# Optimization experiments

Measured on AMD Instinct MI355X. Metric: run time of the kernel, lower is better.

## Reference

```python
import jax, jax.numpy as jnp
import numpy as np


def _leaky(x):
    return jnp.where(x > 0, x, 0.2 * x)


def _time_warp(x, strength, k_wp, k_sh):
    # Vectorized equivalent of the per-sample python loop in _apply_time_warp.
    B, L, Fd = x.shape
    warp_steps = (L * 0.1 * strength).astype(jnp.int32)
    wp = jax.random.randint(k_wp, (B, 1), warp_steps, L - warp_steps)
    sh = jax.random.randint(k_sh, (B, 1), -warp_steps, warp_steps + 1)
    t = jnp.arange(L)[None, :]
    # shift > 0: warped[t] = x[min(t+shift, L-1)] for t >= warp_point, else x[t]
    pos = jnp.where(t >= wp, jnp.minimum(t + sh, L - 1), t)
    # shift < 0: warped[t] = x[t - shift] for warp_point+shift <= t < L+shift, else x[t]
    neg = jnp.where((t >= wp + sh) & (t < L + sh), t - sh, t)
    idx = jnp.where(sh > 0, pos, jnp.where(sh < 0, neg, t))  # (B, L)
    warped = x[jnp.arange(B)[:, None], idx]  # gather along time -> (B, L, Fd)
    return warped


def _freq_aug(x, strength, k_f):
    fx = jnp.fft.fft(x, axis=1)
    ratio = jnp.minimum(strength * 0.1, 0.5)
    keep = jax.random.uniform(k_f, x.shape) > ratio
    res = jnp.fft.ifft(fx * keep.astype(fx.dtype), axis=1).real.astype(x.dtype)
    return jnp.where(strength < 0.01, x, res)


def _forward(x, batch_size, w1, b1, w2, b2, w3, b3, wm, bm, wn, bn, ws, bs,
             p_mask, p_noise, p_shift, p_scale):
    B, L, Fd = x.shape
    s_mask = jax.nn.sigmoid(p_mask)
    s_noise = jax.nn.sigmoid(p_noise)
    s_shift = jax.nn.sigmoid(p_shift)
    s_scale = jax.nn.sigmoid(p_scale)
    s_mix = 1.0 - s_shift

    key = jax.random.key(42)
    kz, kn, kwp, ksh, kf = jax.random.split(key, 5)

    z = jax.random.normal(kz, (B, w1.shape[0]), x.dtype)
    h = _leaky(z @ w1 + b1)
    h = _leaky(h @ w2 + b2)
    h = _leaky(h @ w3 + b3)  # (B, 2*hidden)

    mask = jax.nn.sigmoid(h @ wm + bm).reshape(B, L, Fd)
    mask = 1.0 - (1.0 - mask) * s_mask * 0.3

    noise_mag = jax.nn.softplus(h @ wn + bn).reshape(B, L, Fd)
    noise = jax.random.normal(kn, x.shape, x.dtype) * noise_mag * s_noise * 0.05

    warped = _time_warp(x, s_shift, kwp, ksh)

    scale = jax.nn.softplus(h @ ws + bs)[:, None, :]  # (B,1,Fd)
    scale = 1.0 + (scale - 0.5) * 0.2 * s_scale

    freq = _freq_aug(x, s_mix, kf)

    wa = jnp.clip(1.0 - s_mix - s_shift, 0.1, 0.8)
    wb = s_mix * 0.5
    wc = s_shift * 0.5
    tot = wa + wb + wc
    wa, wb, wc = wa / tot, wb / tot, wc / tot

    aug = x * mask * scale + noise
    aug = aug * wa + freq * wb + warped * wc
    return aug


def setup_inputs() -> dict:
    key = jax.random.key(0)
    ks = jax.random.split(key, 8)
    B, L, Fd = 256, 512, 64
    H, ND = 128, 64
    x = jax.random.normal(ks[0], (B, L, Fd), jnp.float32)

    def lin(k, i, o):
        return jax.random.normal(k, (i, o), jnp.float32) * 0.02

    inp = {
        "x": x,
        "batch_size": B,
        "w1": lin(ks[1], ND, H), "b1": jnp.zeros((H,), jnp.float32),
        "w2": lin(ks[2], H, 2 * H), "b2": jnp.zeros((2 * H,), jnp.float32),
        "w3": lin(ks[3], 2 * H, 2 * H), "b3": jnp.zeros((2 * H,), jnp.float32),
        "wm": lin(ks[4], 2 * H, L * Fd), "bm": jnp.zeros((L * Fd,), jnp.float32),
        "wn": lin(ks[5], 2 * H, L * Fd), "bn": jnp.zeros((L * Fd,), jnp.float32),
        "ws": lin(ks[6], 2 * H, Fd), "bs": jnp.zeros((Fd,), jnp.float32),
        "p_mask": jnp.float32(0.5), "p_noise": jnp.float32(0.5),
        "p_shift": jnp.float32(0.5), "p_scale": jnp.float32(0.5),
    }
    return inp


def reference(x, batch_size, w1, b1, w2, b2, w3, b3, wm, bm, wn, bn, ws, bs,
              p_mask, p_noise, p_shift, p_scale):
    return _forward(x, batch_size, w1, b1, w2, b2, w3, b3, wm, bm, wn, bn,
                    ws, bs, p_mask, p_noise, p_shift, p_scale)
```

## Files before the change

kernel.cpp:

```cpp
#include <hip/hip_runtime.h>
#include <cstdint>
#include <cstddef>


typedef unsigned int u32;
typedef unsigned short u16;

#define Bd 256
#define Ld 512
#define Fd 64
#define Nd 32768

struct U2 { u32 a, b; };

__device__ __forceinline__ u32 rotl32(u32 x, int r){ return (x << r) | (x >> (32 - r)); }

__device__ __forceinline__ U2 tf2x32(u32 k0, u32 k1, u32 x0, u32 x1){
  u32 ks2 = k0 ^ k1 ^ 0x1BD11BDAu;
  x0 += k0; x1 += k1;
#define TFR4(r0,r1,r2,r3) \
  x0 += x1; x1 = rotl32(x1, r0); x1 ^= x0; \
  x0 += x1; x1 = rotl32(x1, r1); x1 ^= x0; \
  x0 += x1; x1 = rotl32(x1, r2); x1 ^= x0; \
  x0 += x1; x1 = rotl32(x1, r3); x1 ^= x0;
  TFR4(13,15,26,6)  x0 += k1;  x1 += ks2 + 1u;
  TFR4(17,29,16,24) x0 += ks2; x1 += k0 + 2u;
  TFR4(13,15,26,6)  x0 += k0;  x1 += k1 + 3u;
  TFR4(17,29,16,24) x0 += k1;  x1 += ks2 + 4u;
  TFR4(13,15,26,6)  x0 += ks2; x1 += k0 + 5u;
#undef TFR4
  U2 r; r.a = x0; r.b = x1; return r;
}

__device__ __forceinline__ u32 rb32(u32 k0, u32 k1, u32 i){
  U2 r = tf2x32(k0, k1, 0u, i);
  return r.a ^ r.b;
}

__device__ __forceinline__ U2 split_key(u32 k0, u32 k1, u32 j){
  return tf2x32(k0, k1, 0u, j);
}

__device__ __forceinline__ float sigmoidf_(float x){ return 1.0f / (1.0f + expf(-x)); }
__device__ __forceinline__ float softplusf_(float x){ return fmaxf(x, 0.0f) + log1pf(expf(-fabsf(x))); }
__device__ __forceinline__ float leakyf_(float x){ return (x > 0.0f) ? x : 0.2f * x; }

__device__ __forceinline__ float erfinvf_(float x){
  float w = -log1pf(-x * x);
  float p;
  if (w < 5.0f){
    w -= 2.5f;
    p =               2.81022636e-08f;
    p = fmaf(p, w,    3.43273939e-07f);
    p = fmaf(p, w,   -3.5233877e-06f);
    p = fmaf(p, w,   -4.39150654e-06f);
    p = fmaf(p, w,    0.00021858087f);
    p = fmaf(p, w,   -0.00125372503f);
    p = fmaf(p, w,   -0.00417768164f);
    p = fmaf(p, w,    0.246640727f);
    p = fmaf(p, w,    1.50140941f);
  } else {
    w = sqrtf(w) - 3.0f;
    p =              -0.000200214257f;
    p = fmaf(p, w,    0.000100950558f);
    p = fmaf(p, w,    0.00134934322f);
    p = fmaf(p, w,   -0.00367342844f);
    p = fmaf(p, w,    0.00573950773f);
    p = fmaf(p, w,   -0.0076224613f);
    p = fmaf(p, w,    0.00943887047f);
    p = fmaf(p, w,    1.00167406f);
    p = fmaf(p, w,    2.83297682f);
  }
  return p * x;
}

__device__ __forceinline__ float uniform_from_bits(u32 bits){
  return __uint_as_float((bits >> 9) | 0x3f800000u) - 1.0f;
}

__device__ __forceinline__ float normal_from_bits(u32 bits){
  float u01 = uniform_from_bits(bits);
  const float lo = -0.99999994f;
  float v = fmaf(u01, 2.0f, lo);
  v = fmaxf(lo, v);
  return 1.41421356f * erfinvf_(v);
}

__device__ __forceinline__ int warp_idx_(int t, int wp, int sh){
  int tps = t + sh;
  int pos = (t >= wp) ? ((tps < Ld - 1) ? tps : (Ld - 1)) : t;
  int neg = ((t >= wp + sh) && (t < Ld + sh)) ? (t - sh) : t;
  return (sh > 0) ? pos : ((sh < 0) ? neg : t);
}

__device__ __forceinline__ u32 pack_bf16_2(float a, float b){
  u32 ua = __float_as_uint(a), ub = __float_as_uint(b);
  u32 ra = (ua + 0x7FFFu + ((ua >> 16) & 1u)) >> 16;
  u32 rb = (ub + 0x7FFFu + ((ub >> 16) & 1u)) >> 16;
  return (ra & 0xFFFFu) | (rb << 16);
}
__device__ __forceinline__ u16 f2bf(float a){
  u32 ua = __float_as_uint(a);
  return (u16)((ua + 0x7FFFu + ((ua >> 16) & 1u)) >> 16);
}
__device__ __forceinline__ float bf2f(u16 v){
  return __uint_as_float(((u32)v) << 16);
}

__device__ __forceinline__ int swz_(int v){
  return ((v >> 2) & 7) ^ ((v & 3) << 1);
}
__device__ __forceinline__ int rev9_(int k){
  return (int)(__brev((u32)k) >> 23);
}

__global__ __launch_bounds__(256) void k_init(float* __restrict__ z, int* __restrict__ wp,
                                              int* __restrict__ shv, const float* __restrict__ p_shift){
  int gid = blockIdx.x * 256 + threadIdx.x;
  U2 kz = split_key(0u, 42u, 0u);
  z[gid] = normal_from_bits(rb32(kz.a, kz.b, (u32)gid));
  if (blockIdx.x == 0){
    int b = threadIdx.x;
    float s_shift = sigmoidf_(p_shift[0]);
    int wsteps = (int)(51.2f * s_shift);
    U2 kwp = split_key(0u, 42u, 2u);
    U2 ksh = split_key(0u, 42u, 3u);
    {
      U2 k1 = split_key(kwp.a, kwp.b, 0u);
      U2 k2 = split_key(kwp.a, kwp.b, 1u);
      u32 hi = rb32(k1.a, k1.b, (u32)b);
      u32 lo = rb32(k2.a, k2.b, (u32)b);
      u32 span = (u32)(Ld - 2 * wsteps);
      u32 mult = 65536u % span; mult = (mult * mult) % span;
      u32 off = ((hi % span) * mult + (lo % span)) % span;
      wp[b] = wsteps + (int)off;
    }
    {
      U2 k1 = split_key(ksh.a, ksh.b, 0u);
      U2 k2 = split_key(ksh.a, ksh.b, 1u);
      u32 hi = rb32(k1.a, k1.b, (u32)b);
      u32 lo = rb32(k2.a, k2.b, (u32)b);
      u32 span = (u32)(2 * wsteps + 1);
      u32 mult = 65536u % span; mult = (mult * mult) % span;
      u32 off = ((hi % span) * mult + (lo % span)) % span;
      shv[b] = -wsteps + (int)off;
    }
  }
}

__global__ __launch_bounds__(128) void k_mlp1(const float* __restrict__ z, const float* __restrict__ w1,
                                              const float* __restrict__ b1, float* __restrict__ h1){
  int b = blockIdx.x, n = threadIdx.x;
  const float* zr = z + b * 64;
  float acc = b1[n];
  #pragma unroll 8
  for (int k = 0; k < 64; ++k) acc = fmaf(zr[k], w1[k * 128 + n], acc);
  h1[b * 128 + n] = leakyf_(acc);
}

__global__ __launch_bounds__(256) void k_mlp2(const float* __restrict__ h1, const float* __restrict__ w2,
                                              const float* __restrict__ b2, float* __restrict__ h2){
  int b = blockIdx.x, n = threadIdx.x;
  const float* hr = h1 + b * 128;
  float acc = b2[n];
  #pragma unroll 8
  for (int k = 0; k < 128; ++k) acc = fmaf(hr[k], w2[k * 256 + n], acc);
  h2[b * 256 + n] = leakyf_(acc);
}

__global__ __launch_bounds__(256) void k_mlp3(const float* __restrict__ h2, const float* __restrict__ w3,
                                              const float* __restrict__ b3, u16* __restrict__ h3b){
  int b = blockIdx.x, n = threadIdx.x;
  const float* hr = h2 + b * 256;
  float acc = b3[n];
  #pragma unroll 8
  for (int k = 0; k < 256; ++k) acc = fmaf(hr[k], w3[k * 256 + n], acc);
  h3b[b * 256 + n] = f2bf(leakyf_(acc));
}

__global__ __launch_bounds__(256) void k_scale(const u16* __restrict__ h3b, const float* __restrict__ wsc,
                                               const float* __restrict__ bsc, const float* __restrict__ p_scale,
                                               float* __restrict__ scl){
  int tid = threadIdx.x;
  int b = blockIdx.x * 4 + (tid >> 6);
  int f = tid & 63;
  float acc = bsc[f];
  for (int k = 0; k < 256; ++k) acc = fmaf(bf2f(h3b[b * 256 + k]), wsc[k * 64 + f], acc);
  float s_scale = sigmoidf_(p_scale[0]);
  scl[b * 64 + f] = 1.0f + (softplusf_(acc) - 0.5f) * 0.2f * s_scale;
}

typedef short short8 __attribute__((ext_vector_type(8)));
typedef float f32x4 __attribute__((ext_vector_type(4)));
union Frag { uint4 u; short8 s; };

__global__ __launch_bounds__(256, 2) void k_gemm(
    const u16* __restrict__ h3b,
    const float* __restrict__ wm, const float* __restrict__ bm,
    const float* __restrict__ wn, const float* __restrict__ bn,
    u16* __restrict__ logM, u16* __restrict__ logN)
{
  __shared__ __align__(16) u32 As [128 * 32];
  __shared__ __align__(16) u32 Bs0[128 * 32];
  __shared__ __align__(16) u32 Bs1[128 * 32];

  const int tid  = threadIdx.x;
  const int lane = tid & 63;
  const int w    = tid >> 6;
  const int q    = lane >> 4;
  const int lo   = lane & 15;
  const int nt0  = blockIdx.x << 7;
  const int b0   = blockIdx.y << 7;
  const int wr   = (w >> 1) << 6;
  const int wc   = (w & 1) << 6;

  const int p  = lane >> 3;
  const int c8 = lane & 7;
  const int nb = (w << 5) + (p << 2);

  f32x4 accm[4][4], accn[4][4];
  #pragma unroll
  for (int i = 0; i < 4; ++i)
    #pragma unroll
    for (int j = 0; j < 4; ++j){ accm[i][j] = (f32x4)0.0f; accn[i][j] = (f32x4)0.0f; }

  for (int kc = 0; kc < 256; kc += 64){
    if (kc) __syncthreads();
    #pragma unroll
    for (int j = 0; j < 4; ++j){
      int idx  = j * 256 + tid;
      int row  = idx >> 3;
      int slot = idx & 7;
      int g    = slot ^ swz_(row);
      uint4 v  = *(const uint4*)(h3b + (size_t)(b0 + row) * 256 + kc + g * 8);
      *(uint4*)&As[row * 32 + slot * 4] = v;
    }
    #pragma unroll
    for (int cp = 0; cp < 4; ++cp){
      int c = cp * 8 + c8;
      size_t gb = (size_t)(kc + 2 * c) * Nd + nt0 + nb;
      float4 m0 = *(const float4*)(wm + gb);
      float4 m1 = *(const float4*)(wm + gb + Nd);
      float4 v0 = *(const float4*)(wn + gb);
      float4 v1 = *(const float4*)(wn + gb + Nd);
      int g = c >> 2, cl = c & 3;
      #pragma unroll
      for (int s = 0; s < 4; ++s){
        int n = nb + s;
        int addr = n * 32 + (g ^ swz_(n)) * 4 + cl;
        float a0 = (s == 0) ? m0.x : (s == 1) ? m0.y : (s == 2) ? m0.z : m0.w;
        float a1 = (s == 0) ? m1.x : (s == 1) ? m1.y : (s == 2) ? m1.z : m1.w;
        float b0f = (s == 0) ? v0.x : (s == 1) ? v0.y : (s == 2) ? v0.z : v0.w;
        float b1f = (s == 0) ? v1.x : (s == 1) ? v1.y : (s == 2) ? v1.z : v1.w;
        Bs0[addr] = pack_bf16_2(a0, a1);
        Bs1[addr] = pack_bf16_2(b0f, b1f);
      }
    }
    __syncthreads();

    #pragma unroll
    for (int u = 0; u < 2; ++u){
      int G = u * 4 + q;
      Frag af[4], bfm[4], bfn[4];
      #pragma unroll
      for (int mt = 0; mt < 4; ++mt){
        int row = wr + mt * 16 + lo;
        af[mt].u = *(const uint4*)&As[row * 32 + (G ^ swz_(row)) * 4];
      }
      #pragma unroll
      for (int nt = 0; nt < 4; ++nt){
        int n = wc + nt * 16 + lo;
        int ad = n * 32 + (G ^ swz_(n)) * 4;
        bfm[nt].u = *(const uint4*)&Bs0[ad];
        bfn[nt].u = *(const uint4*)&Bs1[ad];
      }
      #pragma unroll
      for (int mt = 0; mt < 4; ++mt){
        #pragma unroll
        for (int nt = 0; nt < 4; ++nt){
          accm[mt][nt] = __builtin_amdgcn_mfma_f32_16x16x32_bf16(af[mt].s, bfm[nt].s, accm[mt][nt], 0, 0, 0);
          accn[mt][nt] = __builtin_amdgcn_mfma_f32_16x16x32_bf16(af[mt].s, bfn[nt].s, accn[mt][nt], 0, 0, 0);
        }
      }
    }
  }

  #pragma unroll
  for (int nt = 0; nt < 4; ++nt){
    int n = nt0 + wc + nt * 16 + lo;
    float bmv = bm[n];
    float bnv = bn[n];
    #pragma unroll
    for (int mt = 0; mt < 4; ++mt){
      #pragma unroll
      for (int r = 0; r < 4; ++r){
        int b = b0 + wr + mt * 16 + q * 4 + r;
        size_t o = (size_t)b * Nd + n;
        logM[o] = f2bf(accm[mt][nt][r] + bmv);
        logN[o] = f2bf(accn[mt][nt][r] + bnv);
      }
    }
  }
}

#define PITCH 529

__device__ __forceinline__ int lphys(int t){ return t + (t >> 5); }

__global__ __launch_bounds__(256, 4) void k_faug(
    const float* __restrict__ x,
    const u16* __restrict__ logM, const u16* __restrict__ logN,
    const float* __restrict__ scl,
    const int* __restrict__ wp, const int* __restrict__ shv,
    const float* __restrict__ p_mask, const float* __restrict__ p_noise,
    const float* __restrict__ p_shift,
    float* __restrict__ out)
{
  __shared__ float SR[8 * PITCH];
  __shared__ float SI[8 * PITCH];
  __shared__ float2 tw[256];

  const int tid = threadIdx.x;
  const int b   = blockIdx.x >> 2;
  const int f0  = (blockIdx.x & 3) << 4;

  float s_mask  = sigmoidf_(p_mask[0]);
  float s_noise = sigmoidf_(p_noise[0]);
  float s_shift = sigmoidf_(p_shift[0]);
  float s_mix   = 1.0f - s_shift;
  float ratio   = fminf(s_mix * 0.1f, 0.5f);
  float wa = 1.0f - s_mix - s_shift;
  wa = fminf(fmaxf(wa, 0.1f), 0.8f);
  float wb = s_mix * 0.5f;
  float wc = s_shift * 0.5f;
  float tot = wa + wb + wc;
  wa /= tot; wb /= tot; wc /= tot;
  bool pass = (s_mix < 0.01f);

  U2 kf  = split_key(0u, 42u, 4u);
  U2 knk = split_key(0u, 42u, 1u);
  const int wpb = wp[b];
  const int shb = shv[b];

  {
    float ang = -6.283185307179586f * ((float)tid / 512.0f);
    tw[tid] = make_float2(cosf(ang), sinf(ang));
  }

  const float* xb = x + (size_t)b * Nd;
  #pragma unroll
  for (int s = 0; s < 8; ++s){
    int qq = (s << 8) + tid;
    int t  = qq >> 2;
    int f4 = qq & 3;
    float4 v = *(const float4*)(xb + t * 64 + f0 + (f4 << 2));
    int j = f4 << 1;
    int pt = lphys(t);
    SR[j * PITCH + pt]       = v.x;  SI[j * PITCH + pt]       = v.y;
    SR[(j + 1) * PITCH + pt] = v.z;  SI[(j + 1) * PITCH + pt] = v.w;
  }
  __syncthreads();

  for (int s = 9; s >= 1; --s){
    int half = 1 << (s - 1);
    #pragma unroll
    for (int it = 0; it < 8; ++it){
      int j  = it;
      int bi = tid;
      int pos = bi & (half - 1);
      int g = bi >> (s - 1);
      int i1 = (g << s) + pos;
      int i2 = i1 + half;
      int a1 = j * PITCH + lphys(i1);
      int a2 = j * PITCH + lphys(i2);
      float ur = SR[a1], ui = SI[a1];
      float vr = SR[a2], vi = SI[a2];
      SR[a1] = ur + vr; SI[a1] = ui + vi;
      float dr = ur - vr, di = ui - vi;
      float2 w = tw[pos << (9 - s)];
      SR[a2] = dr * w.x - di * w.y;
      SI[a2] = dr * w.y + di * w.x;
    }
    __syncthreads();
  }

  #pragma unroll
  for (int it = 0; it < 8; ++it){
    int j = it;
    int k = tid;
    int nItr = (k == 0) ? 2 : 1;
    for (int e = 0; e < nItr; ++e){
      int kk = (e == 0) ? k : 256;
      int nk = (512 - kk) & 511;
      int pk = rev9_(kk), pn = rev9_(nk);
      int ak = j * PITCH + lphys(pk);
      int an = j * PITCH + lphys(pn);
      float zkr = SR[ak], zki = SI[ak];
      float znr = SR[an], zni = SI[an];
      float X0r = 0.5f * (zkr + znr), X0i = 0.5f * (zki - zni);
      float X1r = 0.5f * (zki + zni), X1i = 0.5f * (znr - zkr);
      int fA = f0 + (j << 1);
      u32 ck = (u32)((b * Ld + kk) * Fd + fA);
      u32 cn = (u32)((b * Ld + nk) * Fd + fA);
      float k0a = (uniform_from_bits(rb32(kf.a, kf.b, ck))      > ratio) ? 1.0f : 0.0f;
      float k0b = (uniform_from_bits(rb32(kf.a, kf.b, cn))      > ratio) ? 1.0f : 0.0f;
      float k1a = (uniform_from_bits(rb32(kf.a, kf.b, ck + 1u)) > ratio) ? 1.0f : 0.0f;
      float k1b = (uniform_from_bits(rb32(kf.a, kf.b, cn + 1u)) > ratio) ? 1.0f : 0.0f;
      float m0 = 0.5f * (k0a + k0b);
      float m1 = 0.5f * (k1a + k1b);
      SR[ak] = m0 * X0r - m1 * X1i;
      SI[ak] = m0 * X0i + m1 * X1r;
      SR[an] = m0 * X0r + m1 * X1i;
      SI[an] = m1 * X1r - m0 * X0i;
    }
  }
  __syncthreads();

  for (int s = 1; s <= 9; ++s){
    int half = 1 << (s - 1);
    #pragma unroll
    for (int it = 0; it < 8; ++it){
      int j  = it;
      int bi = tid;
      int pos = bi & (half - 1);
      int g = bi >> (s - 1);
      int i1 = (g << s) + pos;
      int i2 = i1 + half;
      int a1 = j * PITCH + lphys(i1);
      int a2 = j * PITCH + lphys(i2);
      float2 w = tw[pos << (9 - s)];
      float vr = SR[a2], vi = SI[a2];
      float tx_ = vr * w.x + vi * w.y;
      float ty_ = vi * w.x - vr * w.y;
      float ur = SR[a1], ui = SI[a1];
      SR[a1] = ur + tx_; SI[a1] = ui + ty_;
      SR[a2] = ur - tx_; SI[a2] = ui - ty_;
    }
    __syncthreads();
  }

  const float inv512 = 1.0f / 512.0f;
  const u16* lMb = logM + (size_t)b * Nd;
  const u16* lNb = logN + (size_t)b * Nd;
  float* ob = out + (size_t)b * Nd;
  #pragma unroll
  for (int s = 0; s < 8; ++s){
    int qq = (s << 8) + tid;
    int t  = qq >> 2;
    int f4 = qq & 3;
    int f  = f0 + (f4 << 2);
    int j  = f4 << 1;
    int pt = lphys(t);
    int nidx = t * 64 + f;
    float4 xv = *(const float4*)(xb + nidx);
    int wi = warp_idx_(t, wpb, shb);
    float4 wv = *(const float4*)(xb + wi * 64 + f);
    float4 sc = *(const float4*)(scl + b * 64 + f);
    ushort4 mr = *(const ushort4*)(lMb + nidx);
    ushort4 nr4 = *(const ushort4*)(lNb + nidx);
    float fr[4];
    fr[0] = SR[j * PITCH + pt] * inv512;
    fr[1] = SI[j * PITCH + pt] * inv512;
    fr[2] = SR[(j + 1) * PITCH + pt] * inv512;
    fr[3] = SI[(j + 1) * PITCH + pt] * inv512;
    const float xvv[4] = {xv.x, xv.y, xv.z, xv.w};
    const float wvv[4] = {wv.x, wv.y, wv.z, wv.w};
    const float scv[4] = {sc.x, sc.y, sc.z, sc.w};
    const u16 mrv[4] = {mr.x, mr.y, mr.z, mr.w};
    const u16 nrv[4] = {nr4.x, nr4.y, nr4.z, nr4.w};
    float o[4];
    #pragma unroll
    for (int c = 0; c < 4; ++c){
      float maskv = sigmoidf_(bf2f(mrv[c]));
      maskv = 1.0f - (1.0f - maskv) * s_mask * 0.3f;
      float nmag = softplusf_(bf2f(nrv[c]));
      float nz = normal_from_bits(rb32(knk.a, knk.b, (u32)(b * Nd + nidx + c)));
      float noise = nz * nmag * s_noise * 0.05f;
      float fq = pass ? xvv[c] : fr[c];
      float aug = fmaf(xvv[c] * maskv, scv[c], noise);
      o[c] = aug * wa + fq * wb + wvv[c] * wc;
    }
    *(float4*)(ob + nidx) = make_float4(o[0], o[1], o[2], o[3]);
  }
}

extern "C" void kernel_launch(void* const* d_in, const int* in_sizes, int n_in,
                              void* d_out, int out_size, void* d_ws, size_t ws_size,
                              hipStream_t stream)
{
  (void)in_sizes; (void)n_in; (void)out_size; (void)ws_size;
  const float* x   = (const float*)d_in[0];
  const float* w1  = (const float*)d_in[2];
  const float* b1  = (const float*)d_in[3];
  const float* w2  = (const float*)d_in[4];
  const float* b2  = (const float*)d_in[5];
  const float* w3  = (const float*)d_in[6];
  const float* b3  = (const float*)d_in[7];
  const float* wm  = (const float*)d_in[8];
  const float* bm  = (const float*)d_in[9];
  const float* wn  = (const float*)d_in[10];
  const float* bn  = (const float*)d_in[11];
  const float* wsc = (const float*)d_in[12];
  const float* bsc = (const float*)d_in[13];
  const float* pm  = (const float*)d_in[14];
  const float* pn  = (const float*)d_in[15];
  const float* psh = (const float*)d_in[16];
  const float* psc = (const float*)d_in[17];
  float* out = (float*)d_out;
  char* ws = (char*)d_ws;

  int*   wp   = (int*)(ws + 0);
  int*   shv  = (int*)(ws + 1024);
  float* z    = (float*)(ws + 2048);
  float* h1   = (float*)(ws + 67584);
  float* h2   = (float*)(ws + 198656);
  u16*   h3b  = (u16*)  (ws + 460800);
  float* scl  = (float*)(ws + 591872);
  u16*   logM = (u16*)  (ws + 1048576);
  u16*   logN = (u16*)  (ws + 1048576 + 16777216);

  k_init <<<dim3(64),      dim3(256), 0, stream>>>(z, wp, shv, psh);
  k_mlp1 <<<dim3(256),     dim3(128), 0, stream>>>(z, w1, b1, h1);
  k_mlp2 <<<dim3(256),     dim3(256), 0, stream>>>(h1, w2, b2, h2);
  k_mlp3 <<<dim3(256),     dim3(256), 0, stream>>>(h2, w3, b3, h3b);
  k_scale<<<dim3(64),      dim3(256), 0, stream>>>(h3b, wsc, bsc, psc, scl);
  k_gemm <<<dim3(256, 2),  dim3(256), 0, stream>>>(h3b, wm, bm, wn, bn, logM, logN);
  k_faug <<<dim3(1024),    dim3(256), 0, stream>>>(x, logM, logN, scl, wp, shv,
                                                   pm, pn, psh, out);
}
```

Baseline: 327.3 us.

## Fuse MLP chain, pre-pack weights to bf16, move mask/noise epilogue into GEMM

```diff
diff --git a/kernel.cpp b/kernel.cpp
--- a/kernel.cpp
+++ b/kernel.cpp
@@ -99,195 +99,205 @@
   u32 rb = (ub + 0x7FFFu + ((ub >> 16) & 1u)) >> 16;
   return (ra & 0xFFFFu) | (rb << 16);
 }
-__device__ __forceinline__ u16 f2bf(float a){
-  u32 ua = __float_as_uint(a);
-  return (u16)((ua + 0x7FFFu + ((ua >> 16) & 1u)) >> 16);
-}
 __device__ __forceinline__ float bf2f(u16 v){
   return __uint_as_float(((u32)v) << 16);
 }
-
-__device__ __forceinline__ int swz_(int v){
-  return ((v >> 2) & 7) ^ ((v & 3) << 1);
-}
 __device__ __forceinline__ int rev9_(int k){
   return (int)(__brev((u32)k) >> 23);
 }
 
-__global__ __launch_bounds__(256) void k_init(float* __restrict__ z, int* __restrict__ wp,
-                                              int* __restrict__ shv, const float* __restrict__ p_shift){
-  int gid = blockIdx.x * 256 + threadIdx.x;
-  U2 kz = split_key(0u, 42u, 0u);
-  z[gid] = normal_from_bits(rb32(kz.a, kz.b, (u32)gid));
-  if (blockIdx.x == 0){
-    int b = threadIdx.x;
+__global__ __launch_bounds__(256) void k_wprep(const float* __restrict__ wm,
+                                               const float* __restrict__ wn,
+                                               u16* __restrict__ wpk){
+  __shared__ float tile[64 * 260];
+  const int mat = blockIdx.x >> 9;
+  const int s   = blockIdx.x & 511;
+  const int t   = threadIdx.x;
+  const float* src = mat ? wn : wm;
+  const size_t matoff = (size_t)mat * 8388608;
+
+  #pragma unroll
+  for (int r = 0; r < 16; ++r){
+    int k  = r * 16 + (t >> 4);
+    int n4 = (t & 15) << 2;
+    float4 v = *(const float4*)(src + (size_t)k * Nd + s * 64 + n4);
+    tile[(n4 + 0) * 260 + k] = v.x;
+    tile[(n4 + 1) * 260 + k] = v.y;
+    tile[(n4 + 2) * 260 + k] = v.z;
+    tile[(n4 + 3) * 260 + k] = v.w;
+  }
+  __syncthreads();
+
+  const int n = t >> 2, part = t & 3;
+  uint4* dst = (uint4*)(wpk + matoff + (size_t)s * 16384 + n * 256 + part * 64);
+  #pragma unroll
+  for (int u = 0; u < 8; ++u){
+    const float* p = &tile[n * 260 + part * 64 + u * 8];
+    uint4 q;
+    q.x = pack_bf16_2(p[0], p[1]); q.y = pack_bf16_2(p[2], p[3]);
+    q.z = pack_bf16_2(p[4], p[5]); q.w = pack_bf16_2(p[6], p[7]);
+    dst[u] = q;
+  }
+}
+
+__global__ __launch_bounds__(256) void k_pre(
+    const float* __restrict__ w1, const float* __restrict__ b1,
+    const float* __restrict__ w2, const float* __restrict__ b2,
+    const float* __restrict__ w3, const float* __restrict__ b3,
+    const float* __restrict__ wsc, const float* __restrict__ bsc,
+    const float* __restrict__ p_shift, const float* __restrict__ p_scale,
+    uint4* __restrict__ h3p, float* __restrict__ scl,
+    int* __restrict__ wp, int* __restrict__ shv)
+{
+  __shared__ float zs[64], h1s[128], h2s[256], h3s[256];
+  const int b = blockIdx.x;
+  const int t = threadIdx.x;
+
+  if (t < 64){
+    U2 kz = split_key(0u, 42u, 0u);
+    zs[t] = normal_from_bits(rb32(kz.a, kz.b, (u32)(b * 64 + t)));
+  }
+  if (t == 64){
     float s_shift = sigmoidf_(p_shift[0]);
     int wsteps = (int)(51.2f * s_shift);
     U2 kwp = split_key(0u, 42u, 2u);
+    U2 k1 = split_key(kwp.a, kwp.b, 0u);
+    U2 k2 = split_key(kwp.a, kwp.b, 1u);
+    u32 hi = rb32(k1.a, k1.b, (u32)b);
+    u32 lo = rb32(k2.a, k2.b, (u32)b);
+    u32 span = (u32)(Ld - 2 * wsteps);
+    u32 mult = 65536u % span; mult = (mult * mult) % span;
+    u32 off = ((hi % span) * mult + (lo % span)) % span;
+    wp[b] = wsteps + (int)off;
+  }
+  if (t == 65){
+    float s_shift = sigmoidf_(p_shift[0]);
+    int wsteps = (int)(51.2f * s_shift);
     U2 ksh = split_key(0u, 42u, 3u);
-    {
-      U2 k1 = split_key(kwp.a, kwp.b, 0u);
-      U2 k2 = split_key(kwp.a, kwp.b, 1u);
-      u32 hi = rb32(k1.a, k1.b, (u32)b);
-      u32 lo = rb32(k2.a, k2.b, (u32)b);
-      u32 span = (u32)(Ld - 2 * wsteps);
-      u32 mult = 65536u % span; mult = (mult * mult) % span;
-      u32 off = ((hi % span) * mult + (lo % span)) % span;
-      wp[b] = wsteps + (int)off;
-    }
-    {
-      U2 k1 = split_key(ksh.a, ksh.b, 0u);
-      U2 k2 = split_key(ksh.a, ksh.b, 1u);
-      u32 hi = rb32(k1.a, k1.b, (u32)b);
-      u32 lo = rb32(k2.a, k2.b, (u32)b);
-      u32 span = (u32)(2 * wsteps + 1);
-      u32 mult = 65536u % span; mult = (mult * mult) % span;
-      u32 off = ((hi % span) * mult + (lo % span)) % span;
-      shv[b] = -wsteps + (int)off;
-    }
-  }
-}
-
-__global__ __launch_bounds__(128) void k_mlp1(const float* __restrict__ z, const float* __restrict__ w1,
-                                              const float* __restrict__ b1, float* __restrict__ h1){
-  int b = blockIdx.x, n = threadIdx.x;
-  const float* zr = z + b * 64;
-  float acc = b1[n];
-  #pragma unroll 8
-  for (int k = 0; k < 64; ++k) acc = fmaf(zr[k], w1[k * 128 + n], acc);
-  h1[b * 128 + n] = leakyf_(acc);
-}
-
-__global__ __launch_bounds__(256) void k_mlp2(const float* __restrict__ h1, const float* __restrict__ w2,
-                                              const float* __restrict__ b2, float* __restrict__ h2){
-  int b = blockIdx.x, n = threadIdx.x;
-  const float* hr = h1 + b * 128;
-  float acc = b2[n];
-  #pragma unroll 8
-  for (int k = 0; k < 128; ++k) acc = fmaf(hr[k], w2[k * 256 + n], acc);
-  h2[b * 256 + n] = leakyf_(acc);
-}
-
-__global__ __launch_bounds__(256) void k_mlp3(const float* __restrict__ h2, const float* __restrict__ w3,
-                                              const float* __restrict__ b3, u16* __restrict__ h3b){
-  int b = blockIdx.x, n = threadIdx.x;
-  const float* hr = h2 + b * 256;
-  float acc = b3[n];
-  #pragma unroll 8
-  for (int k = 0; k < 256; ++k) acc = fmaf(hr[k], w3[k * 256 + n], acc);
-  h3b[b * 256 + n] = f2bf(leakyf_(acc));
-}
-
-__global__ __launch_bounds__(256) void k_scale(const u16* __restrict__ h3b, const float* __restrict__ wsc,
-                                               const float* __restrict__ bsc, const float* __restrict__ p_scale,
-                                               float* __restrict__ scl){
-  int tid = threadIdx.x;
-  int b = blockIdx.x * 4 + (tid >> 6);
-  int f = tid & 63;
-  float acc = bsc[f];
-  for (int k = 0; k < 256; ++k) acc = fmaf(bf2f(h3b[b * 256 + k]), wsc[k * 64 + f], acc);
-  float s_scale = sigmoidf_(p_scale[0]);
-  scl[b * 64 + f] = 1.0f + (softplusf_(acc) - 0.5f) * 0.2f * s_scale;
+    U2 k1 = split_key(ksh.a, ksh.b, 0u);
+    U2 k2 = split_key(ksh.a, ksh.b, 1u);
+    u32 hi = rb32(k1.a, k1.b, (u32)b);
+    u32 lo = rb32(k2.a, k2.b, (u32)b);
+    u32 span = (u32)(2 * wsteps + 1);
+    u32 mult = 65536u % span; mult = (mult * mult) % span;
+    u32 off = ((hi % span) * mult + (lo % span)) % span;
+    shv[b] = -wsteps + (int)off;
+  }
+  __syncthreads();
+
+  if (t < 128){
+    float acc = b1[t];
+    #pragma unroll 8
+    for (int k = 0; k < 64; ++k) acc = fmaf(zs[k], w1[k * 128 + t], acc);
+    h1s[t] = leakyf_(acc);
+  }
+  __syncthreads();
+  {
+    float acc = b2[t];
+    #pragma unroll 8
+    for (int k = 0; k < 128; ++k) acc = fmaf(h1s[k], w2[k * 256 + t], acc);
+    h2s[t] = leakyf_(acc);
+  }
+  __syncthreads();
+  {
+    float acc = b3[t];
+    #pragma unroll 8
+    for (int k = 0; k < 256; ++k) acc = fmaf(h2s[k], w3[k * 256 + t], acc);
+    h3s[t] = leakyf_(acc);
+  }
+  __syncthreads();
+  if (t < 64){
+    float acc = bsc[t];
+    #pragma unroll 8
+    for (int k = 0; k < 256; ++k) acc = fmaf(h3s[k], wsc[k * 64 + t], acc);
+    float s_scale = sigmoidf_(p_scale[0]);
+    scl[b * 64 + t] = 1.0f + (softplusf_(acc) - 0.5f) * 0.2f * s_scale;
+  }
+  if (t < 32){
+    int c = t;
+    int k0 = (c >> 2) * 32 + (c & 3) * 8;
+    uint4 q;
+    q.x = pack_bf16_2(h3s[k0 + 0], h3s[k0 + 1]);
+    q.y = pack_bf16_2(h3s[k0 + 2], h3s[k0 + 3]);
+    q.z = pack_bf16_2(h3s[k0 + 4], h3s[k0 + 5]);
+    q.w = pack_bf16_2(h3s[k0 + 6], h3s[k0 + 7]);
+    h3p[(b >> 4) * 512 + c * 16 + (b & 15)] = q;
+  }
 }
 
 typedef short short8 __attribute__((ext_vector_type(8)));
 typedef float f32x4 __attribute__((ext_vector_type(4)));
 union Frag { uint4 u; short8 s; };
 
-__global__ __launch_bounds__(256, 2) void k_gemm(
-    const u16* __restrict__ h3b,
-    const float* __restrict__ wm, const float* __restrict__ bm,
-    const float* __restrict__ wn, const float* __restrict__ bn,
-    u16* __restrict__ logM, u16* __restrict__ logN)
+__global__ __launch_bounds__(256) void k_gemm2(
+    const uint4* __restrict__ h3p, const u16* __restrict__ wpk,
+    const float* __restrict__ bm, const float* __restrict__ bn,
+    const float* __restrict__ scl,
+    const float* __restrict__ p_mask, const float* __restrict__ p_noise,
+    u32* __restrict__ mno)
 {
-  __shared__ __align__(16) u32 As [128 * 32];
-  __shared__ __align__(16) u32 Bs0[128 * 32];
-  __shared__ __align__(16) u32 Bs1[128 * 32];
+  __shared__ __align__(16) uint4 Bs[4096];
 
   const int tid  = threadIdx.x;
   const int lane = tid & 63;
   const int w    = tid >> 6;
   const int q    = lane >> 4;
   const int lo   = lane & 15;
-  const int nt0  = blockIdx.x << 7;
+  const int bx   = blockIdx.x;
   const int b0   = blockIdx.y << 7;
-  const int wr   = (w >> 1) << 6;
-  const int wc   = (w & 1) << 6;
-
-  const int p  = lane >> 3;
-  const int c8 = lane & 7;
-  const int nb = (w << 5) + (p << 2);
-
-  f32x4 accm[4][4], accn[4][4];
+  const int wr   = (w & 1) << 6;
+  const int wc   = (w >> 1) << 5;
+
+  #pragma unroll
+  for (int i = 0; i < 16; ++i){
+    int slot = i * 256 + tid;
+    int mat  = slot >> 11;
+    int np   = (slot >> 5) & 63;
+    int gp   = slot & 31;
+    int gi   = gp ^ (np & 7);
+    Bs[slot] = *(const uint4*)(wpk + (size_t)mat * 8388608 +
+                               (size_t)bx * 16384 + np * 256 + gi * 8);
+  }
+  __syncthreads();
+
+  f32x4 accm[4][2], accn[4][2];
   #pragma unroll
   for (int i = 0; i < 4; ++i)
     #pragma unroll
-    for (int j = 0; j < 4; ++j){ accm[i][j] = (f32x4)0.0f; accn[i][j] = (f32x4)0.0f; }
-
-  for (int kc = 0; kc < 256; kc += 64){
-    if (kc) __syncthreads();
-    #pragma unroll
-    for (int j = 0; j < 4; ++j){
-      int idx  = j * 256 + tid;
-      int row  = idx >> 3;
-      int slot = idx & 7;
-      int g    = slot ^ swz_(row);
-      uint4 v  = *(const uint4*)(h3b + (size_t)(b0 + row) * 256 + kc + g * 8);
-      *(uint4*)&As[row * 32 + slot * 4] = v;
-    }
-    #pragma unroll
-    for (int cp = 0; cp < 4; ++cp){
-      int c = cp * 8 + c8;
-      size_t gb = (size_t)(kc + 2 * c) * Nd + nt0 + nb;
-      float4 m0 = *(const float4*)(wm + gb);
-      float4 m1 = *(const float4*)(wm + gb + Nd);
-      float4 v0 = *(const float4*)(wn + gb);
-      float4 v1 = *(const float4*)(wn + gb + Nd);
-      int g = c >> 2, cl = c & 3;
+    for (int j = 0; j < 2; ++j){ accm[i][j] = (f32x4)0.0f; accn[i][j] = (f32x4)0.0f; }
+
+  const int tbase = (blockIdx.y << 3) + ((w & 1) << 2);
+
+  for (int G = 0; G < 8; ++G){
+    Frag af[4], bfm[2], bfn[2];
+    #pragma unroll
+    for (int mt = 0; mt < 4; ++mt)
+      af[mt].u = h3p[(tbase + mt) * 512 + (G * 4 + q) * 16 + lo];
+    #pragma unroll
+    for (int nt = 0; nt < 2; ++nt){
+      int np = wc + nt * 16 + lo;
+      int gp = (G * 4 + q) ^ (np & 7);
+      bfm[nt].u = Bs[np * 32 + gp];
+      bfn[nt].u = Bs[2048 + np * 32 + gp];
+    }
+    #pragma unroll
+    for (int mt = 0; mt < 4; ++mt){
       #pragma unroll
-      for (int s = 0; s < 4; ++s){
-        int n = nb + s;
-        int addr = n * 32 + (g ^ swz_(n)) * 4 + cl;
-        float a0 = (s == 0) ? m0.x : (s == 1) ? m0.y : (s == 2) ? m0.z : m0.w;
-        float a1 = (s == 0) ? m1.x : (s == 1) ? m1.y : (s == 2) ? m1.z : m1.w;
-        float b0f = (s == 0) ? v0.x : (s == 1) ? v0.y : (s == 2) ? v0.z : v0.w;
-        float b1f = (s == 0) ? v1.x : (s == 1) ? v1.y : (s == 2) ? v1.z : v1.w;
-        Bs0[addr] = pack_bf16_2(a0, a1);
-        Bs1[addr] = pack_bf16_2(b0f, b1f);
+      for (int nt = 0; nt < 2; ++nt){
+        accm[mt][nt] = __builtin_amdgcn_mfma_f32_16x16x32_bf16(af[mt].s, bfm[nt].s, accm[mt][nt], 0, 0, 0);
+        accn[mt][nt] = __builtin_amdgcn_mfma_f32_16x16x32_bf16(af[mt].s, bfn[nt].s, accn[mt][nt], 0, 0, 0);
       }
     }
-    __syncthreads();
-
-    #pragma unroll
-    for (int u = 0; u < 2; ++u){
-      int G = u * 4 + q;
-      Frag af[4], bfm[4], bfn[4];
-      #pragma unroll
-      for (int mt = 0; mt < 4; ++mt){
-        int row = wr + mt * 16 + lo;
-        af[mt].u = *(const uint4*)&As[row * 32 + (G ^ swz_(row)) * 4];
-      }
-      #pragma unroll
-      for (int nt = 0; nt < 4; ++nt){
-        int n = wc + nt * 16 + lo;
-        int ad = n * 32 + (G ^ swz_(n)) * 4;
-        bfm[nt].u = *(const uint4*)&Bs0[ad];
-        bfn[nt].u = *(const uint4*)&Bs1[ad];
-      }
-      #pragma unroll
-      for (int mt = 0; mt < 4; ++mt){
-        #pragma unroll
-        for (int nt = 0; nt < 4; ++nt){
-          accm[mt][nt] = __builtin_amdgcn_mfma_f32_16x16x32_bf16(af[mt].s, bfm[nt].s, accm[mt][nt], 0, 0, 0);
-          accn[mt][nt] = __builtin_amdgcn_mfma_f32_16x16x32_bf16(af[mt].s, bfn[nt].s, accn[mt][nt], 0, 0, 0);
-        }
-      }
-    }
-  }
-
-  #pragma unroll
-  for (int nt = 0; nt < 4; ++nt){
-    int n = nt0 + wc + nt * 16 + lo;
+  }
+
+  float s_mask  = sigmoidf_(p_mask[0]);
+  float s_noise = sigmoidf_(p_noise[0]);
+  U2 knk = split_key(0u, 42u, 1u);
+
+  #pragma unroll
+  for (int nt = 0; nt < 2; ++nt){
+    int f = wc + nt * 16 + lo;
+    int n = (bx << 6) + f;
     float bmv = bm[n];
     float bnv = bn[n];
     #pragma unroll
@@ -295,24 +305,25 @@
       #pragma unroll
       for (int r = 0; r < 4; ++r){
         int b = b0 + wr + mt * 16 + q * 4 + r;
-        size_t o = (size_t)b * Nd + n;
-        logM[o] = f2bf(accm[mt][nt][r] + bmv);
-        logN[o] = f2bf(accn[mt][nt][r] + bnv);
+        float maskv = sigmoidf_(accm[mt][nt][r] + bmv);
+        maskv = 1.0f - (1.0f - maskv) * s_mask * 0.3f;
+        float mne = maskv * scl[b * 64 + (n & 63)];
+        float nmag = softplusf_(accn[mt][nt][r] + bnv);
+        float nz = normal_from_bits(rb32(knk.a, knk.b, (u32)(b * Nd + n)));
+        float noise = nz * nmag * s_noise * 0.05f;
+        mno[(size_t)b * Nd + n] = pack_bf16_2(mne, noise);
       }
     }
   }
 }
 
 #define PITCH 529
-
 __device__ __forceinline__ int lphys(int t){ return t + (t >> 5); }
 
-__global__ __launch_bounds__(256, 4) void k_faug(
+__global__ __launch_bounds__(256, 4) void k_faug2(
     const float* __restrict__ x,
-    const u16* __restrict__ logM, const u16* __restrict__ logN,
-    const float* __restrict__ scl,
+    const u32* __restrict__ mno,
     const int* __restrict__ wp, const int* __restrict__ shv,
-    const float* __restrict__ p_mask, const float* __restrict__ p_noise,
     const float* __restrict__ p_shift,
     float* __restrict__ out)
 {
@@ -324,8 +335,6 @@
   const int b   = blockIdx.x >> 2;
   const int f0  = (blockIdx.x & 3) << 4;
 
-  float s_mask  = sigmoidf_(p_mask[0]);
-  float s_noise = sigmoidf_(p_noise[0]);
   float s_shift = sigmoidf_(p_shift[0]);
   float s_mix   = 1.0f - s_shift;
   float ratio   = fminf(s_mix * 0.1f, 0.5f);
@@ -337,8 +346,7 @@
   wa /= tot; wb /= tot; wc /= tot;
   bool pass = (s_mix < 0.01f);
 
-  U2 kf  = split_key(0u, 42u, 4u);
-  U2 knk = split_key(0u, 42u, 1u);
+  U2 kf = split_key(0u, 42u, 4u);
   const int wpb = wp[b];
   const int shb = shv[b];
 
@@ -377,9 +385,9 @@
       float vr = SR[a2], vi = SI[a2];
       SR[a1] = ur + vr; SI[a1] = ui + vi;
       float dr = ur - vr, di = ui - vi;
-      float2 w = tw[pos << (9 - s)];
-      SR[a2] = dr * w.x - di * w.y;
-      SI[a2] = dr * w.y + di * w.x;
+      float2 wv = tw[pos << (9 - s)];
+      SR[a2] = dr * wv.x - di * wv.y;
+      SI[a2] = dr * wv.y + di * wv.x;
     }
     __syncthreads();
   }
@@ -428,10 +436,10 @@
       int i2 = i1 + half;
       int a1 = j * PITCH + lphys(i1);
       int a2 = j * PITCH + lphys(i2);
-      float2 w = tw[pos << (9 - s)];
+      float2 wv = tw[pos << (9 - s)];
       float vr = SR[a2], vi = SI[a2];
-      float tx_ = vr * w.x + vi * w.y;
-      float ty_ = vi * w.x - vr * w.y;
+      float tx_ = vr * wv.x + vi * wv.y;
+      float ty_ = vi * wv.x - vr * wv.y;
       float ur = SR[a1], ui = SI[a1];
       SR[a1] = ur + tx_; SI[a1] = ui + ty_;
       SR[a2] = ur - tx_; SI[a2] = ui - ty_;
@@ -440,8 +448,7 @@
   }
 
   const float inv512 = 1.0f / 512.0f;
-  const u16* lMb = logM + (size_t)b * Nd;
-  const u16* lNb = logN + (size_t)b * Nd;
+  const u32* mb = mno + (size_t)b * Nd;
   float* ob = out + (size_t)b * Nd;
   #pragma unroll
   for (int s = 0; s < 8; ++s){
@@ -455,9 +462,7 @@
     float4 xv = *(const float4*)(xb + nidx);
     int wi = warp_idx_(t, wpb, shb);
     float4 wv = *(const float4*)(xb + wi * 64 + f);
-    float4 sc = *(const float4*)(scl + b * 64 + f);
-    ushort4 mr = *(const ushort4*)(lMb + nidx);
-    ushort4 nr4 = *(const ushort4*)(lNb + nidx);
+    uint4 mv = *(const uint4*)(mb + nidx);
     float fr[4];
     fr[0] = SR[j * PITCH + pt] * inv512;
     fr[1] = SI[j * PITCH + pt] * inv512;
@@ -465,19 +470,14 @@
     fr[3] = SI[(j + 1) * PITCH + pt] * inv512;
     const float xvv[4] = {xv.x, xv.y, xv.z, xv.w};
     const float wvv[4] = {wv.x, wv.y, wv.z, wv.w};
-    const float scv[4] = {sc.x, sc.y, sc.z, sc.w};
-    const u16 mrv[4] = {mr.x, mr.y, mr.z, mr.w};
-    const u16 nrv[4] = {nr4.x, nr4.y, nr4.z, nr4.w};
+    const u32 mvv[4] = {mv.x, mv.y, mv.z, mv.w};
     float o[4];
     #pragma unroll
     for (int c = 0; c < 4; ++c){
-      float maskv = sigmoidf_(bf2f(mrv[c]));
-      maskv = 1.0f - (1.0f - maskv) * s_mask * 0.3f;
-      float nmag = softplusf_(bf2f(nrv[c]));
-      float nz = normal_from_bits(rb32(knk.a, knk.b, (u32)(b * Nd + nidx + c)));
-      float noise = nz * nmag * s_noise * 0.05f;
+      float mne = bf2f((u16)(mvv[c] & 0xFFFFu));
+      float noi = bf2f((u16)(mvv[c] >> 16));
+      float aug = fmaf(xvv[c], mne, noi);
       float fq = pass ? xvv[c] : fr[c];
-      float aug = fmaf(xvv[c] * maskv, scv[c], noise);
       o[c] = aug * wa + fq * wb + wvv[c] * wc;
     }
     *(float4*)(ob + nidx) = make_float4(o[0], o[1], o[2], o[3]);
@@ -509,22 +509,16 @@
   float* out = (float*)d_out;
   char* ws = (char*)d_ws;
 
-  int*   wp   = (int*)(ws + 0);
-  int*   shv  = (int*)(ws + 1024);
-  float* z    = (float*)(ws + 2048);
-  float* h1   = (float*)(ws + 67584);
-  float* h2   = (float*)(ws + 198656);
-  u16*   h3b  = (u16*)  (ws + 460800);
-  float* scl  = (float*)(ws + 591872);
-  u16*   logM = (u16*)  (ws + 1048576);
-  u16*   logN = (u16*)  (ws + 1048576 + 16777216);
-
-  k_init <<<dim3(64),      dim3(256), 0, stream>>>(z, wp, shv, psh);
-  k_mlp1 <<<dim3(256),     dim3(128), 0, stream>>>(z, w1, b1, h1);
-  k_mlp2 <<<dim3(256),     dim3(256), 0, stream>>>(h1, w2, b2, h2);
-  k_mlp3 <<<dim3(256),     dim3(256), 0, stream>>>(h2, w3, b3, h3b);
-  k_scale<<<dim3(64),      dim3(256), 0, stream>>>(h3b, wsc, bsc, psc, scl);
-  k_gemm <<<dim3(256, 2),  dim3(256), 0, stream>>>(h3b, wm, bm, wn, bn, logM, logN);
-  k_faug <<<dim3(1024),    dim3(256), 0, stream>>>(x, logM, logN, scl, wp, shv,
-                                                   pm, pn, psh, out);
-}
+  int*   wp   = (int*)  (ws + 0);
+  int*   shv  = (int*)  (ws + 1024);
+  float* scl  = (float*)(ws + 2048);
+  uint4* h3p  = (uint4*)(ws + 67584);
+  u32*   mno  = (u32*)  (ws + 1048576);
+  u16*   wpk  = (u16*)d_out;
+
+  k_wprep<<<dim3(1024),   dim3(256), 0, stream>>>(wm, wn, wpk);
+  k_pre  <<<dim3(256),    dim3(256), 0, stream>>>(w1, b1, w2, b2, w3, b3, wsc, bsc,
+                                                  psh, psc, h3p, scl, wp, shv);
+  k_gemm2<<<dim3(512, 2), dim3(256), 0, stream>>>(h3p, wpk, bm, bn, scl, pm, pn, mno);
+  k_faug2<<<dim3(1024),   dim3(256), 0, stream>>>(x, mno, wp, shv, psh, out);
+}
```

Measured after the change: 348.8 us. +6.6%, slower.
